# Performance work log

Hardware: AMD Instinct MI355X
Metric: run time of the kernel (lower is better)

The kernel has to match this reference:

```python
import jax, jax.numpy as jnp
import numpy as np

N_NODES = 100000
N_EDGES = 1600000
IN_CH = 128
HID = 64


def gcn_conv(x, W, b, src, dst, n):
    """PyG-style GCNConv: add self-loops, symmetric deg^-1/2 normalization."""
    h = x @ W  # [n, out]
    # degree including self-loop, computed from destination (col) indices
    deg = jax.ops.segment_sum(jnp.ones_like(dst, dtype=h.dtype), dst, num_segments=n) + 1.0
    dinv = jax.lax.rsqrt(deg)  # [n]
    norm = dinv[src] * dinv[dst]  # [E]
    agg = jax.ops.segment_sum(h[src] * norm[:, None], dst, num_segments=n)
    agg = agg + h * (1.0 / deg)[:, None]  # self-loop term: norm = 1/deg
    return agg + b


def setup_inputs() -> dict:
    key = jax.random.key(0)
    ks = jax.random.split(key, 6)
    x = jax.random.normal(ks[0], (N_NODES, IN_CH), dtype=jnp.float32)
    edge_index = jax.random.randint(ks[1], (2, N_EDGES), 0, N_NODES, dtype=jnp.int64)
    W1 = jax.random.normal(ks[2], (IN_CH, HID), dtype=jnp.float32) / np.sqrt(IN_CH)
    b1 = jnp.zeros((HID,), dtype=jnp.float32)
    W2 = jax.random.normal(ks[3], (HID, HID), dtype=jnp.float32) / np.sqrt(HID)
    b2 = jnp.zeros((HID,), dtype=jnp.float32)
    Wl = jax.random.normal(ks[4], (HID, 1), dtype=jnp.float32) / np.sqrt(HID)
    bl = jnp.zeros((1,), dtype=jnp.float32)
    return {"x": x, "edge_index": edge_index, "W1": W1, "b1": b1,
            "W2": W2, "b2": b2, "Wl": Wl, "bl": bl}


def reference(x, edge_index, W1, b1, W2, b2, Wl, bl):
    src, dst = edge_index[0], edge_index[1]
    n = x.shape[0]
    h = gcn_conv(x, W1, b1, src, dst, n)
    h = jax.nn.relu(h)
    # dropout: identity in eval mode
    h = gcn_conv(h, W2, b2, src, dst, n)
    h = jax.nn.relu(h)
    out = (h @ Wl + bl)[:, 0]  # [n]
    return out
```

## Files before the change

kernel.cpp:

```cpp
#include <hip/hip_runtime.h>
#include <hip/hip_fp16.h>


#define SHIFT 9
#define BSZ   (1 << SHIFT)
#define NBMAX 256
#define BIN_CH 1024
#define PMAX  11776

using f16x8 = __attribute__((ext_vector_type(8))) _Float16;
using f16x2 = __attribute__((ext_vector_type(2))) _Float16;
using f32x4 = __attribute__((ext_vector_type(4))) float;

__global__ __launch_bounds__(256) void k_bin(const int* __restrict__ src,
                                             const int* __restrict__ dst,
                                             unsigned* __restrict__ binned,
                                             int* __restrict__ gbase,
                                             __half* __restrict__ hs,
                                             int n, int nb, int E) {
    if (blockIdx.x == 0 && threadIdx.x < 8) {
        uint4 z = {0u, 0u, 0u, 0u};
        reinterpret_cast<uint4*>(hs + ((size_t)n << 6))[threadIdx.x] = z;
    }
    __shared__ int h[NBMAX];
    __shared__ int ex[NBMAX + 1];
    __shared__ int cur[NBMAX];
    __shared__ int stmp[256];
    const int t = threadIdx.x;
    const int blk = blockIdx.x;
    const int beg = blk * BIN_CH;
    for (int i = t; i < NBMAX; i += 256) h[i] = 0;
    __syncthreads();
    const int e4 = beg + t * 4;
    const bool act = e4 < E;
    int4 d4 = {0, 0, 0, 0};
    if (act) {
        d4 = *reinterpret_cast<const int4*>(dst + e4);
        atomicAdd(&h[d4.x >> SHIFT], 1);
        atomicAdd(&h[d4.y >> SHIFT], 1);
        atomicAdd(&h[d4.z >> SHIFT], 1);
        atomicAdd(&h[d4.w >> SHIFT], 1);
    }
    __syncthreads();
    const int hv = (t < nb) ? h[t] : 0;
    stmp[t] = hv;
    __syncthreads();
    for (int off = 1; off < 256; off <<= 1) {
        int u = (t >= off) ? stmp[t - off] : 0;
        __syncthreads();
        stmp[t] += u;
        __syncthreads();
    }
    if (t <= nb) ex[t] = stmp[t] - ((t < nb) ? h[t] : 0);
    __syncthreads();
    if (t < nb) cur[t] = ex[t];
    if (t <= nb) gbase[(size_t)blk * (nb + 1) + t] = ex[t];
    __syncthreads();
    if (act) {
        const int4 s4 = *reinterpret_cast<const int4*>(src + e4);
        int b0 = d4.x >> SHIFT, b1 = d4.y >> SHIFT;
        int b2 = d4.z >> SHIFT, b3 = d4.w >> SHIFT;
        int p0 = atomicAdd(&cur[b0], 1);
        int p1 = atomicAdd(&cur[b1], 1);
        int p2 = atomicAdd(&cur[b2], 1);
        int p3 = atomicAdd(&cur[b3], 1);
        binned[beg + p0] = (unsigned)s4.x | ((unsigned)(d4.x & (BSZ - 1)) << 17);
        binned[beg + p1] = (unsigned)s4.y | ((unsigned)(d4.y & (BSZ - 1)) << 17);
        binned[beg + p2] = (unsigned)s4.z | ((unsigned)(d4.z & (BSZ - 1)) << 17);
        binned[beg + p3] = (unsigned)s4.w | ((unsigned)(d4.w & (BSZ - 1)) << 17);
    }
}

#define TD 32
__global__ __launch_bounds__(256) void k_xpose(const int* __restrict__ gbase,
                                               int* __restrict__ gbaseT,
                                               int nblk, int nbp1) {
    __shared__ int tile[TD][TD + 1];
    const int ctiles = (nbp1 + TD - 1) / TD;
    const int bx = blockIdx.x % ctiles;
    const int by = blockIdx.x / ctiles;
    const int c0 = bx * TD, r0 = by * TD;
    const int tx = threadIdx.x & 31, ty = threadIdx.x >> 5;
    for (int dy = ty; dy < TD; dy += 8) {
        int r = r0 + dy, c = c0 + tx;
        tile[dy][tx] = (r < nblk && c < nbp1) ? gbase[(size_t)r * nbp1 + c] : 0;
    }
    __syncthreads();
    for (int dy = ty; dy < TD; dy += 8) {
        int r = c0 + dy, c = r0 + tx;
        if (r < nbp1 && c < nblk)
            gbaseT[(size_t)r * nblk + c] = tile[tx][dy];
    }
}

__global__ __launch_bounds__(1024) void k_bfill(const unsigned* __restrict__ binned,
                                                const int* __restrict__ gbaseT,
                                                int nblk, int nb,
                                                int* __restrict__ rowptr,
                                                int* __restrict__ colidx,
                                                float* __restrict__ dinv, int n) {
    __shared__ unsigned pedges[PMAX];
    __shared__ int segarr[2048];
    __shared__ int stmp[1024];
    __shared__ int cnt[BSZ];
    __shared__ int nbase[BSZ];
    const int b = blockIdx.x;
    const int t = threadIdx.x;
    const int* rowS = gbaseT + (size_t)b * nblk;
    const int* rowE = gbaseT + (size_t)(b + 1) * nblk;
    for (int i = t; i < BSZ; i += 1024) cnt[i] = 0;
    int eb = 0;
    {
        int l0 = 0, l1 = 0;
        if (t < nblk)        { int s0 = rowS[t];        l0 = rowE[t] - s0;        eb += s0; }
        if (t + 1024 < nblk) { int s0 = rowS[t + 1024]; l1 = rowE[t + 1024] - s0; eb += s0; }
        segarr[t] = l0;
        segarr[t + 1024] = l1;
    }
    stmp[t] = eb;
    __syncthreads();
    for (int off = 512; off; off >>= 1) {
        if (t < off) stmp[t] += stmp[t + off];
        __syncthreads();
    }
    const int ebeg = stmp[0];
    __syncthreads();
    const int a0 = segarr[2 * t];
    const int a1 = segarr[2 * t + 1];
    const int ps = a0 + a1;
    stmp[t] = ps;
    __syncthreads();
    for (int off = 1; off < 1024; off <<= 1) {
        int u = (t >= off) ? stmp[t - off] : 0;
        __syncthreads();
        stmp[t] += u;
        __syncthreads();
    }
    const int ecnt = min(stmp[1023], PMAX);
    const int exp2_ = stmp[t] - ps;
    segarr[2 * t] = exp2_;
    segarr[2 * t + 1] = exp2_ + a0;
    __syncthreads();
    for (int blk = t; blk < nblk; blk += 1024) {
        const int s0 = rowS[blk];
        const int c = rowE[blk] - s0;
        const int pos = segarr[blk];
        const unsigned* bp = binned + (size_t)blk * BIN_CH + s0;
        for (int k = 0; k < c; ++k) {
            const int d = pos + k;
            if (d < PMAX) pedges[d] = bp[k];
        }
    }
    __syncthreads();
    for (int j = t; j < ecnt; j += 1024)
        atomicAdd(&cnt[pedges[j] >> 17], 1);
    __syncthreads();
    const int c0 = (t < 256) ? cnt[2 * t] : 0;
    const int c1 = (t < 256) ? cnt[2 * t + 1] : 0;
    const int s2 = c0 + c1;
    stmp[t] = s2;
    __syncthreads();
    for (int off = 1; off < 256; off <<= 1) {
        int u = (t >= off && t < 256) ? stmp[t - off] : 0;
        __syncthreads();
        if (t < 256) stmp[t] += u;
        __syncthreads();
    }
    if (t < 256) {
        const int ex = stmp[t] - s2;
        nbase[2 * t] = ex;
        nbase[2 * t + 1] = ex + c0;
    }
    __syncthreads();
    const int gb9 = b << SHIFT;
    for (int j = t; j < BSZ; j += 1024) {
        const int g = gb9 + j;
        if (g < n) {
            rowptr[g] = (int)(((unsigned)(ebeg + nbase[j]) << 8) |
                              (unsigned)min(cnt[j], 255));
            dinv[g] = rsqrtf((float)cnt[j] + 1.0f);
        }
        cnt[j] = nbase[j];
    }
    __syncthreads();
    for (int j = t; j < ecnt; j += 1024) {
        const unsigned e = pedges[j];
        const int lo = (int)(e >> 17);
        const int off = atomicAdd(&cnt[lo], 1);
        colidx[ebeg + off] = (int)((e & 0x1FFFFu) << 7);
    }
}

template <int K, bool A_FP32>
__global__ __launch_bounds__(256) void k_gemm_mfma(const void* __restrict__ Av,
                                                   const float* __restrict__ W,
                                                   const float* __restrict__ dinv,
                                                   __half* __restrict__ C, int n) {
    constexpr int KP = K + 8;
    __shared__ _Float16 Wt[64 * KP];
    const int tid = threadIdx.x;
    for (int i = tid; i < K * 64; i += 256) {
        int k = i >> 6, c = i & 63;
        Wt[c * KP + k] = (_Float16)W[i];
    }
    __syncthreads();

    const int lane = tid & 63;
    const int wv = tid >> 6;
    const int r16 = lane & 15;
    const int kq = lane >> 4;
    const int rb = blockIdx.x * 64 + wv * 16;
    const int arow = min(rb + r16, n - 1);

    f32x4 acc[4] = {{0.f,0.f,0.f,0.f},{0.f,0.f,0.f,0.f},
                    {0.f,0.f,0.f,0.f},{0.f,0.f,0.f,0.f}};

#pragma unroll
    for (int kk = 0; kk < K; kk += 32) {
        f16x8 a;
        if (A_FP32) {
            const float* Ap = (const float*)Av + (size_t)arow * K + kk + kq * 8;
            float4 f0 = *reinterpret_cast<const float4*>(Ap);
            float4 f1 = *reinterpret_cast<const float4*>(Ap + 4);
            a[0] = (_Float16)f0.x; a[1] = (_Float16)f0.y;
            a[2] = (_Float16)f0.z; a[3] = (_Float16)f0.w;
            a[4] = (_Float16)f1.x; a[5] = (_Float16)f1.y;
            a[6] = (_Float16)f1.z; a[7] = (_Float16)f1.w;
        } else {
            const _Float16* Ap = (const _Float16*)Av + (size_t)arow * K + kk + kq * 8;
            a = *reinterpret_cast<const f16x8*>(Ap);
        }
#pragma unroll
        for (int nt = 0; nt < 4; ++nt) {
            f16x8 b = *reinterpret_cast<const f16x8*>(&Wt[(nt * 16 + r16) * KP + kk + kq * 8]);
            acc[nt] = __builtin_amdgcn_mfma_f32_16x16x32_f16(a, b, acc[nt], 0, 0, 0);
        }
    }

#pragma unroll
    for (int r = 0; r < 4; ++r) {
        const int row = rb + kq * 4 + r;
        if (row < n) {
            const float di = dinv[row];
#pragma unroll
            for (int nt = 0; nt < 4; ++nt)
                C[((size_t)row << 6) + nt * 16 + r16] = __float2half(acc[nt][r] * di);
        }
    }
}

__device__ __forceinline__ void dotu4(float acc[8], uint4 u, f16x2 pl, f16x2 ph) {
    union { uint4 u4; f16x2 h[4]; } v;
    v.u4 = u;
    acc[0] = __builtin_amdgcn_fdot2(v.h[0], pl, acc[0], false);
    acc[1] = __builtin_amdgcn_fdot2(v.h[0], ph, acc[1], false);
    acc[2] = __builtin_amdgcn_fdot2(v.h[1], pl, acc[2], false);
    acc[3] = __builtin_amdgcn_fdot2(v.h[1], ph, acc[3], false);
    acc[4] = __builtin_amdgcn_fdot2(v.h[2], pl, acc[4], false);
    acc[5] = __builtin_amdgcn_fdot2(v.h[2], ph, acc[5], false);
    acc[6] = __builtin_amdgcn_fdot2(v.h[3], pl, acc[6], false);
    acc[7] = __builtin_amdgcn_fdot2(v.h[3], ph, acc[7], false);
}

__device__ __forceinline__ void fold8(float acc[8]) {
#pragma unroll
    for (int m = 8; m <= 32; m <<= 1) {
#pragma unroll
        for (int j = 0; j < 8; ++j)
            acc[j] += __shfl_xor(acc[j], m, 64);
    }
}

__device__ __forceinline__ void gather_pair(const char* __restrict__ hsb,
                                            const int* __restrict__ colidx,
                                            unsigned pk0, unsigned pk1,
                                            int g, int p, unsigned dum,
                                            float acc0[8], float acc1[8]) {
    const f16x2 pl = {(_Float16)1.0f, (_Float16)0.0f};
    const f16x2 ph = {(_Float16)0.0f, (_Float16)1.0f};
    const int beg0 = (int)(pk0 >> 8), deg0 = (int)(pk0 & 255u);
    const int beg1 = (int)(pk1 >> 8), deg1 = (int)(pk1 & 255u);
    const int t0 = deg0 - g, t1 = deg1 - g;
    const unsigned poff = (unsigned)(p << 4);
    const unsigned dumo = dum + poff;
    const int ia = beg0 + g;
    const int ib = beg1 + g;
    unsigned a0 = (unsigned)colidx[ia]      + poff;
    unsigned a1 = (unsigned)colidx[ia + 8]  + poff;
    unsigned a2 = (unsigned)colidx[ia + 16] + poff;
    unsigned a3 = (unsigned)colidx[ia + 24] + poff;
    unsigned b0 = (unsigned)colidx[ib]      + poff;
    unsigned b1 = (unsigned)colidx[ib + 8]  + poff;
    unsigned b2 = (unsigned)colidx[ib + 16] + poff;
    unsigned b3 = (unsigned)colidx[ib + 24] + poff;
    unsigned oa0 = (0  < t0) ? a0 : dumo;
    unsigned oa1 = (8  < t0) ? a1 : dumo;
    unsigned oa2 = (16 < t0) ? a2 : dumo;
    unsigned oa3 = (24 < t0) ? a3 : dumo;
    unsigned ob0 = (0  < t1) ? b0 : dumo;
    unsigned ob1 = (8  < t1) ? b1 : dumo;
    unsigned ob2 = (16 < t1) ? b2 : dumo;
    unsigned ob3 = (24 < t1) ? b3 : dumo;
    uint4 ua0 = *reinterpret_cast<const uint4*>(hsb + oa0);
    uint4 ua1 = *reinterpret_cast<const uint4*>(hsb + oa1);
    uint4 ua2 = *reinterpret_cast<const uint4*>(hsb + oa2);
    uint4 ua3 = *reinterpret_cast<const uint4*>(hsb + oa3);
    uint4 ub0 = *reinterpret_cast<const uint4*>(hsb + ob0);
    uint4 ub1 = *reinterpret_cast<const uint4*>(hsb + ob1);
    uint4 ub2 = *reinterpret_cast<const uint4*>(hsb + ob2);
    uint4 ub3 = *reinterpret_cast<const uint4*>(hsb + ob3);
    dotu4(acc0, ua0, pl, ph);
    dotu4(acc0, ua1, pl, ph);
    dotu4(acc0, ua2, pl, ph);
    dotu4(acc0, ua3, pl, ph);
    dotu4(acc1, ub0, pl, ph);
    dotu4(acc1, ub1, pl, ph);
    dotu4(acc1, ub2, pl, ph);
    dotu4(acc1, ub3, pl, ph);
    const int ns0 = (deg0 + 7) >> 3;
    for (int k = 4; k < ns0; k += 4) {
        const int ik = beg0 + 8 * k + g;
        unsigned c0 = (unsigned)colidx[ik]      + poff;
        unsigned c1 = (unsigned)colidx[ik + 8]  + poff;
        unsigned c2 = (unsigned)colidx[ik + 16] + poff;
        unsigned c3 = (unsigned)colidx[ik + 24] + poff;
        const int kb = 8 * k;
        uint4 u0 = *reinterpret_cast<const uint4*>(hsb + ((kb      < t0) ? c0 : dumo));
        uint4 u1 = *reinterpret_cast<const uint4*>(hsb + ((kb + 8  < t0) ? c1 : dumo));
        uint4 u2 = *reinterpret_cast<const uint4*>(hsb + ((kb + 16 < t0) ? c2 : dumo));
        uint4 u3 = *reinterpret_cast<const uint4*>(hsb + ((kb + 24 < t0) ? c3 : dumo));
        dotu4(acc0, u0, pl, ph);
        dotu4(acc0, u1, pl, ph);
        dotu4(acc0, u2, pl, ph);
        dotu4(acc0, u3, pl, ph);
    }
    const int ns1 = (deg1 + 7) >> 3;
    for (int k = 4; k < ns1; k += 4) {
        const int ik = beg1 + 8 * k + g;
        unsigned c0 = (unsigned)colidx[ik]      + poff;
        unsigned c1 = (unsigned)colidx[ik + 8]  + poff;
        unsigned c2 = (unsigned)colidx[ik + 16] + poff;
        unsigned c3 = (unsigned)colidx[ik + 24] + poff;
        const int kb = 8 * k;
        uint4 u0 = *reinterpret_cast<const uint4*>(hsb + ((kb      < t1) ? c0 : dumo));
        uint4 u1 = *reinterpret_cast<const uint4*>(hsb + ((kb + 8  < t1) ? c1 : dumo));
        uint4 u2 = *reinterpret_cast<const uint4*>(hsb + ((kb + 16 < t1) ? c2 : dumo));
        uint4 u3 = *reinterpret_cast<const uint4*>(hsb + ((kb + 24 < t1) ? c3 : dumo));
        dotu4(acc1, u0, pl, ph);
        dotu4(acc1, u1, pl, ph);
        dotu4(acc1, u2, pl, ph);
        dotu4(acc1, u3, pl, ph);
    }
    fold8(acc0);
    fold8(acc1);
}

__global__ __launch_bounds__(256) void k_agg_relu(const __half* __restrict__ hs,
                                                  const int* __restrict__ rowptr,
                                                  const int* __restrict__ colidx,
                                                  const float* __restrict__ dinv,
                                                  const float* __restrict__ b,
                                                  __half* __restrict__ out, int n) {
    const int wv = threadIdx.x >> 6;
    const int i0 = blockIdx.x * 8 + wv * 2;
    const int lane = threadIdx.x & 63;
    if (i0 >= n) return;
    const int i1 = min(i0 + 1, n - 1);
    const int g = lane >> 3, p = lane & 7;
    const int iw = (lane & 8) ? i1 : i0;
    const unsigned pk0 = (unsigned)rowptr[i0];
    const unsigned pk1 = (unsigned)rowptr[i1];
    uint4 su = *reinterpret_cast<const uint4*>(hs + ((size_t)iw << 6) + (p << 3));
    const float di = dinv[iw];
    float acc0[8] = {}, acc1[8] = {};
    gather_pair((const char*)hs, colidx, pk0, pk1, g, p, (unsigned)n << 7,
                acc0, acc1);
    if (lane < 16) {
        const f16x2 pl = {(_Float16)1.0f, (_Float16)0.0f};
        const f16x2 ph = {(_Float16)0.0f, (_Float16)1.0f};
        float a[8];
#pragma unroll
        for (int j = 0; j < 8; ++j) a[j] = (lane & 8) ? acc1[j] : acc0[j];
        dotu4(a, su, pl, ph);
        float4 b0 = *reinterpret_cast<const float4*>(b + (p << 3));
        float4 b1 = *reinterpret_cast<const float4*>(b + (p << 3) + 4);
        __half2 h0 = __halves2half2(__float2half(fmaxf(fmaf(a[0], di, b0.x), 0.f)),
                                    __float2half(fmaxf(fmaf(a[1], di, b0.y), 0.f)));
        __half2 h1 = __halves2half2(__float2half(fmaxf(fmaf(a[2], di, b0.z), 0.f)),
                                    __float2half(fmaxf(fmaf(a[3], di, b0.w), 0.f)));
        __half2 h2 = __halves2half2(__float2half(fmaxf(fmaf(a[4], di, b1.x), 0.f)),
                                    __float2half(fmaxf(fmaf(a[5], di, b1.y), 0.f)));
        __half2 h3 = __halves2half2(__float2half(fmaxf(fmaf(a[6], di, b1.z), 0.f)),
                                    __float2half(fmaxf(fmaf(a[7], di, b1.w), 0.f)));
        uint4 u;
        u.x = *reinterpret_cast<unsigned*>(&h0);
        u.y = *reinterpret_cast<unsigned*>(&h1);
        u.z = *reinterpret_cast<unsigned*>(&h2);
        u.w = *reinterpret_cast<unsigned*>(&h3);
        if (iw < n && (i0 + 1 < n || !(lane & 8)))
            *reinterpret_cast<uint4*>(out + ((size_t)iw << 6) + (p << 3)) = u;
    }
}

__global__ __launch_bounds__(256) void k_agg_head(const __half* __restrict__ hs,
                                                  const int* __restrict__ rowptr,
                                                  const int* __restrict__ colidx,
                                                  const float* __restrict__ dinv,
                                                  const float* __restrict__ b2,
                                                  const float* __restrict__ Wl,
                                                  const float* __restrict__ bl,
                                                  float* __restrict__ out, int n) {
    const int wv = threadIdx.x >> 6;
    const int i0 = blockIdx.x * 8 + wv * 2;
    const int lane = threadIdx.x & 63;
    if (i0 >= n) return;
    const int i1 = min(i0 + 1, n - 1);
    const int g = lane >> 3, p = lane & 7;
    const int iw = (lane & 8) ? i1 : i0;
    const unsigned pk0 = (unsigned)rowptr[i0];
    const unsigned pk1 = (unsigned)rowptr[i1];
    uint4 su = *reinterpret_cast<const uint4*>(hs + ((size_t)iw << 6) + (p << 3));
    const float di = dinv[iw];
    float acc0[8] = {}, acc1[8] = {};
    gather_pair((const char*)hs, colidx, pk0, pk1, g, p, (unsigned)n << 7,
                acc0, acc1);
    const f16x2 pl = {(_Float16)1.0f, (_Float16)0.0f};
    const f16x2 ph = {(_Float16)0.0f, (_Float16)1.0f};
    float a[8];
#pragma unroll
    for (int j = 0; j < 8; ++j) a[j] = (lane & 8) ? acc1[j] : acc0[j];
    dotu4(a, su, pl, ph);
    float4 b0 = *reinterpret_cast<const float4*>(b2 + (p << 3));
    float4 b1 = *reinterpret_cast<const float4*>(b2 + (p << 3) + 4);
    float4 w0 = *reinterpret_cast<const float4*>(Wl + (p << 3));
    float4 w1 = *reinterpret_cast<const float4*>(Wl + (p << 3) + 4);
    float v = fmaxf(fmaf(a[0], di, b0.x), 0.f) * w0.x
            + fmaxf(fmaf(a[1], di, b0.y), 0.f) * w0.y
            + fmaxf(fmaf(a[2], di, b0.z), 0.f) * w0.z
            + fmaxf(fmaf(a[3], di, b0.w), 0.f) * w0.w
            + fmaxf(fmaf(a[4], di, b1.x), 0.f) * w1.x
            + fmaxf(fmaf(a[5], di, b1.y), 0.f) * w1.y
            + fmaxf(fmaf(a[6], di, b1.z), 0.f) * w1.z
            + fmaxf(fmaf(a[7], di, b1.w), 0.f) * w1.w;
    v += __shfl_xor(v, 1, 64);
    v += __shfl_xor(v, 2, 64);
    v += __shfl_xor(v, 4, 64);
    if (lane == 0) out[i0] = v + bl[0];
    if (lane == 8 && i0 + 1 < n) out[i1] = v + bl[0];
}

extern "C" void kernel_launch(void* const* d_in, const int* in_sizes, int n_in,
                              void* d_out, int out_size, void* d_ws, size_t ws_size,
                              hipStream_t stream) {
    const float* x  = (const float*)d_in[0];
    const int*   ei = (const int*)d_in[1];
    const float* W1 = (const float*)d_in[2];
    const float* b1 = (const float*)d_in[3];
    const float* W2 = (const float*)d_in[4];
    const float* b2 = (const float*)d_in[5];
    const float* Wl = (const float*)d_in[6];
    const float* bl = (const float*)d_in[7];
    float* out = (float*)d_out;

    const int n = in_sizes[0] / 128;
    const int E = in_sizes[1] / 2;
    const int* src = ei;
    const int* dst = ei + E;
    const int nb = (n + BSZ - 1) >> SHIFT;
    const int nblk = (E + BIN_CH - 1) / BIN_CH;

    char* ws = (char*)d_ws;
    size_t o = 0;
    auto alloc = [&](size_t bytes) {
        void* p = ws + o;
        o = (o + bytes + 255) & ~(size_t)255;
        return p;
    };
    float* dinv    = (float*)alloc((size_t)n * 4);
    int*   rowptr  = (int*)  alloc((size_t)(n + 1) * 4);
    int*   colidx  = (int*)  alloc(((size_t)E + 64) * 4);
    int*   gbase   = (int*)  alloc((size_t)nblk * (nb + 1) * 4);
    int*   gbaseT  = (int*)  alloc((size_t)(nb + 1) * nblk * 4);
    __half* hs     = (__half*)alloc((size_t)(n + 1) * 64 * 2);
    __half* bufA   = (__half*)alloc((size_t)n * 64 * 2);
    unsigned* binned = (unsigned*)alloc(((size_t)nblk * BIN_CH) * 4);

    k_bin<<<nblk, 256, 0, stream>>>(src, dst, binned, gbase, hs, n, nb, E);
    const int ctiles = (nb + 1 + TD - 1) / TD;
    const int rtiles = (nblk + TD - 1) / TD;
    k_xpose<<<ctiles * rtiles, 256, 0, stream>>>(gbase, gbaseT, nblk, nb + 1);
    k_bfill<<<nb, 1024, 0, stream>>>(binned, gbaseT, nblk, nb, rowptr, colidx,
                                     dinv, n);

    k_gemm_mfma<128, true><<<(n + 63) / 64, 256, 0, stream>>>(x, W1, dinv, hs, n);
    k_agg_relu<<<(n + 7) / 8, 256, 0, stream>>>(hs, rowptr, colidx, dinv, b1, bufA, n);

    k_gemm_mfma<64, false><<<(n + 63) / 64, 256, 0, stream>>>(bufA, W2, dinv, hs, n);
    k_agg_head<<<(n + 7) / 8, 256, 0, stream>>>(hs, rowptr, colidx, dinv, b2, Wl, bl,
                                                out, n);
}
```

Baseline: 133.1 us.

## Split aggregation by degree class, packing four low-degree nodes per wavefront

While building the CSR, nodes are classified into low-degree (<=16) and high-degree lists. Separate aggregation kernels then handle low-degree nodes four per wavefront, each with two gather slots per lane group, and high-degree nodes two per wavefront as before. The aim is to reduce wasted lanes and idle gather iterations for the many nodes with average degree around 16. The cost is extra global atomics and list writes in k_bfill, indirect node indexing that scatters output writes, and two more kernel launches sized for the worst case, whose extra blocks exit early.

```diff
diff --git a/kernel.cpp b/kernel.cpp
--- a/kernel.cpp
+++ b/kernel.cpp
@@ -17,10 +17,12 @@
                                              unsigned* __restrict__ binned,
                                              int* __restrict__ gbase,
                                              __half* __restrict__ hs,
+                                             int* __restrict__ clscnt,
                                              int n, int nb, int E) {
     if (blockIdx.x == 0 && threadIdx.x < 8) {
         uint4 z = {0u, 0u, 0u, 0u};
         reinterpret_cast<uint4*>(hs + ((size_t)n << 6))[threadIdx.x] = z;
+        if (threadIdx.x < 2) clscnt[threadIdx.x] = 0;
     }
     __shared__ int h[NBMAX];
     __shared__ int ex[NBMAX + 1];
@@ -98,17 +100,22 @@
                                                 int nblk, int nb,
                                                 int* __restrict__ rowptr,
                                                 int* __restrict__ colidx,
-                                                float* __restrict__ dinv, int n) {
+                                                float* __restrict__ dinv,
+                                                int* __restrict__ list0,
+                                                int* __restrict__ list1,
+                                                int* __restrict__ clscnt, int n) {
     __shared__ unsigned pedges[PMAX];
     __shared__ int segarr[2048];
     __shared__ int stmp[1024];
     __shared__ int cnt[BSZ];
     __shared__ int nbase[BSZ];
+    __shared__ int lcnt[2], lcur[2], lbase[2];
     const int b = blockIdx.x;
     const int t = threadIdx.x;
     const int* rowS = gbaseT + (size_t)b * nblk;
     const int* rowE = gbaseT + (size_t)(b + 1) * nblk;
     for (int i = t; i < BSZ; i += 1024) cnt[i] = 0;
+    if (t < 2) lcnt[t] = 0;
     int eb = 0;
     {
         int l0 = 0, l1 = 0;
@@ -176,9 +183,26 @@
     for (int j = t; j < BSZ; j += 1024) {
         const int g = gb9 + j;
         if (g < n) {
+            const int dg = cnt[j];
             rowptr[g] = (int)(((unsigned)(ebeg + nbase[j]) << 8) |
-                              (unsigned)min(cnt[j], 255));
-            dinv[g] = rsqrtf((float)cnt[j] + 1.0f);
+                              (unsigned)min(dg, 255));
+            dinv[g] = rsqrtf((float)dg + 1.0f);
+            atomicAdd(&lcnt[dg <= 16 ? 0 : 1], 1);
+        }
+    }
+    __syncthreads();
+    if (t < 2) {
+        lbase[t] = atomicAdd(&clscnt[t], lcnt[t]);
+        lcur[t] = 0;
+    }
+    __syncthreads();
+    for (int j = t; j < BSZ; j += 1024) {
+        const int g = gb9 + j;
+        if (g < n) {
+            const int dg = cnt[j];
+            const int c = dg <= 16 ? 0 : 1;
+            const int pos = atomicAdd(&lcur[c], 1);
+            (c ? list1 : list0)[lbase[c] + pos] = g;
         }
         cnt[j] = nbase[j];
     }
@@ -355,81 +379,96 @@
     fold8(acc1);
 }
 
-__global__ __launch_bounds__(256) void k_agg_relu(const __half* __restrict__ hs,
-                                                  const int* __restrict__ rowptr,
-                                                  const int* __restrict__ colidx,
-                                                  const float* __restrict__ dinv,
-                                                  const float* __restrict__ b,
-                                                  __half* __restrict__ out, int n) {
-    const int wv = threadIdx.x >> 6;
-    const int i0 = blockIdx.x * 8 + wv * 2;
-    const int lane = threadIdx.x & 63;
-    if (i0 >= n) return;
-    const int i1 = min(i0 + 1, n - 1);
-    const int g = lane >> 3, p = lane & 7;
-    const int iw = (lane & 8) ? i1 : i0;
-    const unsigned pk0 = (unsigned)rowptr[i0];
-    const unsigned pk1 = (unsigned)rowptr[i1];
-    uint4 su = *reinterpret_cast<const uint4*>(hs + ((size_t)iw << 6) + (p << 3));
-    const float di = dinv[iw];
-    float acc0[8] = {}, acc1[8] = {};
-    gather_pair((const char*)hs, colidx, pk0, pk1, g, p, (unsigned)n << 7,
-                acc0, acc1);
-    if (lane < 16) {
-        const f16x2 pl = {(_Float16)1.0f, (_Float16)0.0f};
-        const f16x2 ph = {(_Float16)0.0f, (_Float16)1.0f};
-        float a[8];
-#pragma unroll
-        for (int j = 0; j < 8; ++j) a[j] = (lane & 8) ? acc1[j] : acc0[j];
-        dotu4(a, su, pl, ph);
-        float4 b0 = *reinterpret_cast<const float4*>(b + (p << 3));
-        float4 b1 = *reinterpret_cast<const float4*>(b + (p << 3) + 4);
-        __half2 h0 = __halves2half2(__float2half(fmaxf(fmaf(a[0], di, b0.x), 0.f)),
-                                    __float2half(fmaxf(fmaf(a[1], di, b0.y), 0.f)));
-        __half2 h1 = __halves2half2(__float2half(fmaxf(fmaf(a[2], di, b0.z), 0.f)),
-                                    __float2half(fmaxf(fmaf(a[3], di, b0.w), 0.f)));
-        __half2 h2 = __halves2half2(__float2half(fmaxf(fmaf(a[4], di, b1.x), 0.f)),
-                                    __float2half(fmaxf(fmaf(a[5], di, b1.y), 0.f)));
-        __half2 h3 = __halves2half2(__float2half(fmaxf(fmaf(a[6], di, b1.z), 0.f)),
-                                    __float2half(fmaxf(fmaf(a[7], di, b1.w), 0.f)));
-        uint4 u;
-        u.x = *reinterpret_cast<unsigned*>(&h0);
-        u.y = *reinterpret_cast<unsigned*>(&h1);
-        u.z = *reinterpret_cast<unsigned*>(&h2);
-        u.w = *reinterpret_cast<unsigned*>(&h3);
-        if (iw < n && (i0 + 1 < n || !(lane & 8)))
-            *reinterpret_cast<uint4*>(out + ((size_t)iw << 6) + (p << 3)) = u;
-    }
-}
-
-__global__ __launch_bounds__(256) void k_agg_head(const __half* __restrict__ hs,
-                                                  const int* __restrict__ rowptr,
-                                                  const int* __restrict__ colidx,
-                                                  const float* __restrict__ dinv,
-                                                  const float* __restrict__ b2,
-                                                  const float* __restrict__ Wl,
-                                                  const float* __restrict__ bl,
-                                                  float* __restrict__ out, int n) {
-    const int wv = threadIdx.x >> 6;
-    const int i0 = blockIdx.x * 8 + wv * 2;
-    const int lane = threadIdx.x & 63;
-    if (i0 >= n) return;
-    const int i1 = min(i0 + 1, n - 1);
-    const int g = lane >> 3, p = lane & 7;
-    const int iw = (lane & 8) ? i1 : i0;
-    const unsigned pk0 = (unsigned)rowptr[i0];
-    const unsigned pk1 = (unsigned)rowptr[i1];
-    uint4 su = *reinterpret_cast<const uint4*>(hs + ((size_t)iw << 6) + (p << 3));
-    const float di = dinv[iw];
-    float acc0[8] = {}, acc1[8] = {};
-    gather_pair((const char*)hs, colidx, pk0, pk1, g, p, (unsigned)n << 7,
-                acc0, acc1);
+__device__ __forceinline__ void gather_quad2(const char* __restrict__ hsb,
+                                             const int* __restrict__ colidx,
+                                             unsigned pk0, unsigned pk1,
+                                             unsigned pk2, unsigned pk3,
+                                             int g, int p, unsigned dum,
+                                             float a0[8], float a1[8],
+                                             float a2[8], float a3[8]) {
     const f16x2 pl = {(_Float16)1.0f, (_Float16)0.0f};
     const f16x2 ph = {(_Float16)0.0f, (_Float16)1.0f};
-    float a[8];
-#pragma unroll
-    for (int j = 0; j < 8; ++j) a[j] = (lane & 8) ? acc1[j] : acc0[j];
-    dotu4(a, su, pl, ph);
+    const int beg0 = (int)(pk0 >> 8), deg0 = (int)(pk0 & 255u);
+    const int beg1 = (int)(pk1 >> 8), deg1 = (int)(pk1 & 255u);
+    const int beg2 = (int)(pk2 >> 8), deg2 = (int)(pk2 & 255u);
+    const int beg3 = (int)(pk3 >> 8), deg3 = (int)(pk3 & 255u);
+    const int t0 = deg0 - g, t1 = deg1 - g, t2 = deg2 - g, t3 = deg3 - g;
+    const unsigned poff = (unsigned)(p << 4);
+    const unsigned dumo = dum + poff;
+    const int ia = beg0 + g, ib = beg1 + g, ic = beg2 + g, id = beg3 + g;
+    unsigned a_0 = (unsigned)colidx[ia]     + poff;
+    unsigned a_1 = (unsigned)colidx[ia + 8] + poff;
+    unsigned b_0 = (unsigned)colidx[ib]     + poff;
+    unsigned b_1 = (unsigned)colidx[ib + 8] + poff;
+    unsigned c_0 = (unsigned)colidx[ic]     + poff;
+    unsigned c_1 = (unsigned)colidx[ic + 8] + poff;
+    unsigned d_0 = (unsigned)colidx[id]     + poff;
+    unsigned d_1 = (unsigned)colidx[id + 8] + poff;
+    unsigned oa0 = (0 < t0) ? a_0 : dumo;
+    unsigned oa1 = (8 < t0) ? a_1 : dumo;
+    unsigned ob0 = (0 < t1) ? b_0 : dumo;
+    unsigned ob1 = (8 < t1) ? b_1 : dumo;
+    unsigned oc0 = (0 < t2) ? c_0 : dumo;
+    unsigned oc1 = (8 < t2) ? c_1 : dumo;
+    unsigned od0 = (0 < t3) ? d_0 : dumo;
+    unsigned od1 = (8 < t3) ? d_1 : dumo;
+    uint4 ua0 = *reinterpret_cast<const uint4*>(hsb + oa0);
+    uint4 ua1 = *reinterpret_cast<const uint4*>(hsb + oa1);
+    uint4 ub0 = *reinterpret_cast<const uint4*>(hsb + ob0);
+    uint4 ub1 = *reinterpret_cast<const uint4*>(hsb + ob1);
+    uint4 uc0 = *reinterpret_cast<const uint4*>(hsb + oc0);
+    uint4 uc1 = *reinterpret_cast<const uint4*>(hsb + oc1);
+    uint4 ud0 = *reinterpret_cast<const uint4*>(hsb + od0);
+    uint4 ud1 = *reinterpret_cast<const uint4*>(hsb + od1);
+    dotu4(a0, ua0, pl, ph);
+    dotu4(a0, ua1, pl, ph);
+    dotu4(a1, ub0, pl, ph);
+    dotu4(a1, ub1, pl, ph);
+    dotu4(a2, uc0, pl, ph);
+    dotu4(a2, uc1, pl, ph);
+    dotu4(a3, ud0, pl, ph);
+    dotu4(a3, ud1, pl, ph);
+    fold8(a0);
+    fold8(a1);
+    fold8(a2);
+    fold8(a3);
+}
+
+__device__ __forceinline__ void sel4(float a[8], int nsel, const float a0[8],
+                                     const float a1[8], const float a2[8],
+                                     const float a3[8]) {
+#pragma unroll
+    for (int j = 0; j < 8; ++j) {
+        float x01 = (nsel & 1) ? a1[j] : a0[j];
+        float x23 = (nsel & 1) ? a3[j] : a2[j];
+        a[j] = (nsel & 2) ? x23 : x01;
+    }
+}
+
+__device__ __forceinline__ void store_relu(float a[8], float di,
+                                           const float* __restrict__ b, int p,
+                                           __half* __restrict__ out, int row) {
+    float4 b0 = *reinterpret_cast<const float4*>(b + (p << 3));
+    float4 b1 = *reinterpret_cast<const float4*>(b + (p << 3) + 4);
+    __half2 h0 = __halves2half2(__float2half(fmaxf(fmaf(a[0], di, b0.x), 0.f)),
+                                __float2half(fmaxf(fmaf(a[1], di, b0.y), 0.f)));
+    __half2 h1 = __halves2half2(__float2half(fmaxf(fmaf(a[2], di, b0.z), 0.f)),
+                                __float2half(fmaxf(fmaf(a[3], di, b0.w), 0.f)));
+    __half2 h2 = __halves2half2(__float2half(fmaxf(fmaf(a[4], di, b1.x), 0.f)),
+                                __float2half(fmaxf(fmaf(a[5], di, b1.y), 0.f)));
+    __half2 h3 = __halves2half2(__float2half(fmaxf(fmaf(a[6], di, b1.z), 0.f)),
+                                __float2half(fmaxf(fmaf(a[7], di, b1.w), 0.f)));
+    uint4 u;
+    u.x = *reinterpret_cast<unsigned*>(&h0);
+    u.y = *reinterpret_cast<unsigned*>(&h1);
+    u.z = *reinterpret_cast<unsigned*>(&h2);
+    u.w = *reinterpret_cast<unsigned*>(&h3);
+    *reinterpret_cast<uint4*>(out + ((size_t)row << 6) + (p << 3)) = u;
+}
+
+__device__ __forceinline__ float head_val(float a[8], float di,
+                                          const float* __restrict__ b2,
+                                          const float* __restrict__ Wl, int p) {
     float4 b0 = *reinterpret_cast<const float4*>(b2 + (p << 3));
     float4 b1 = *reinterpret_cast<const float4*>(b2 + (p << 3) + 4);
     float4 w0 = *reinterpret_cast<const float4*>(Wl + (p << 3));
@@ -445,8 +484,162 @@
     v += __shfl_xor(v, 1, 64);
     v += __shfl_xor(v, 2, 64);
     v += __shfl_xor(v, 4, 64);
-    if (lane == 0) out[i0] = v + bl[0];
-    if (lane == 8 && i0 + 1 < n) out[i1] = v + bl[0];
+    return v;
+}
+
+__global__ __launch_bounds__(256) void k_agg_relu_c0(const __half* __restrict__ hs,
+                                                     const int* __restrict__ rowptr,
+                                                     const int* __restrict__ colidx,
+                                                     const int* __restrict__ list,
+                                                     const int* __restrict__ clscnt,
+                                                     const float* __restrict__ dinv,
+                                                     const float* __restrict__ b,
+                                                     __half* __restrict__ out, int n) {
+    const int cntc = clscnt[0];
+    const int i0 = (blockIdx.x * 4 + (threadIdx.x >> 6)) * 4;
+    if (i0 >= cntc) return;
+    const int lane = threadIdx.x & 63;
+    const int g = lane >> 3, p = lane & 7;
+    const int nsel = g & 3;
+    const int last = cntc - 1;
+    const int id0 = list[min(i0,     last)];
+    const int id1 = list[min(i0 + 1, last)];
+    const int id2 = list[min(i0 + 2, last)];
+    const int id3 = list[min(i0 + 3, last)];
+    const int idsel = (nsel & 1) ? ((nsel & 2) ? id3 : id1)
+                                 : ((nsel & 2) ? id2 : id0);
+    const bool valid = (i0 + nsel) < cntc;
+    const unsigned pk0 = (unsigned)rowptr[id0];
+    const unsigned pk1 = (unsigned)rowptr[id1];
+    const unsigned pk2 = (unsigned)rowptr[id2];
+    const unsigned pk3 = (unsigned)rowptr[id3];
+    uint4 su = *reinterpret_cast<const uint4*>(hs + ((size_t)idsel << 6) + (p << 3));
+    const float di = dinv[idsel];
+    float a0[8] = {}, a1[8] = {}, a2[8] = {}, a3[8] = {};
+    gather_quad2((const char*)hs, colidx, pk0, pk1, pk2, pk3, g, p,
+                 (unsigned)n << 7, a0, a1, a2, a3);
+    if (lane < 32 && valid) {
+        const f16x2 pl = {(_Float16)1.0f, (_Float16)0.0f};
+        const f16x2 ph = {(_Float16)0.0f, (_Float16)1.0f};
+        float a[8];
+        sel4(a, nsel, a0, a1, a2, a3);
+        dotu4(a, su, pl, ph);
+        store_relu(a, di, b, p, out, idsel);
+    }
+}
+
+__global__ __launch_bounds__(256) void k_agg_relu_c1(const __half* __restrict__ hs,
+                                                     const int* __restrict__ rowptr,
+                                                     const int* __restrict__ colidx,
+                                                     const int* __restrict__ list,
+                                                     const int* __restrict__ clscnt,
+                                                     const float* __restrict__ dinv,
+                                                     const float* __restrict__ b,
+                                                     __half* __restrict__ out, int n) {
+    const int cntc = clscnt[1];
+    const int i0 = (blockIdx.x * 4 + (threadIdx.x >> 6)) * 2;
+    if (i0 >= cntc) return;
+    const int lane = threadIdx.x & 63;
+    const int g = lane >> 3, p = lane & 7;
+    const int last = cntc - 1;
+    const int id0 = list[min(i0,     last)];
+    const int id1 = list[min(i0 + 1, last)];
+    const int iw = (lane & 8) ? id1 : id0;
+    const bool valid = (i0 + ((lane >> 3) & 1)) < cntc;
+    const unsigned pk0 = (unsigned)rowptr[id0];
+    const unsigned pk1 = (unsigned)rowptr[id1];
+    uint4 su = *reinterpret_cast<const uint4*>(hs + ((size_t)iw << 6) + (p << 3));
+    const float di = dinv[iw];
+    float acc0[8] = {}, acc1[8] = {};
+    gather_pair((const char*)hs, colidx, pk0, pk1, g, p, (unsigned)n << 7,
+                acc0, acc1);
+    if (lane < 16 && valid) {
+        const f16x2 pl = {(_Float16)1.0f, (_Float16)0.0f};
+        const f16x2 ph = {(_Float16)0.0f, (_Float16)1.0f};
+        float a[8];
+#pragma unroll
+        for (int j = 0; j < 8; ++j) a[j] = (lane & 8) ? acc1[j] : acc0[j];
+        dotu4(a, su, pl, ph);
+        store_relu(a, di, b, p, out, iw);
+    }
+}
+
+__global__ __launch_bounds__(256) void k_agg_head_c0(const __half* __restrict__ hs,
+                                                     const int* __restrict__ rowptr,
+                                                     const int* __restrict__ colidx,
+                                                     const int* __restrict__ list,
+                                                     const int* __restrict__ clscnt,
+                                                     const float* __restrict__ dinv,
+                                                     const float* __restrict__ b2,
+                                                     const float* __restrict__ Wl,
+                                                     const float* __restrict__ bl,
+                                                     float* __restrict__ out, int n) {
+    const int cntc = clscnt[0];
+    const int i0 = (blockIdx.x * 4 + (threadIdx.x >> 6)) * 4;
+    if (i0 >= cntc) return;
+    const int lane = threadIdx.x & 63;
+    const int g = lane >> 3, p = lane & 7;
+    const int nsel = g & 3;
+    const int last = cntc - 1;
+    const int id0 = list[min(i0,     last)];
+    const int id1 = list[min(i0 + 1, last)];
+    const int id2 = list[min(i0 + 2, last)];
+    const int id3 = list[min(i0 + 3, last)];
+    const int idsel = (nsel & 1) ? ((nsel & 2) ? id3 : id1)
+                                 : ((nsel & 2) ? id2 : id0);
+    const unsigned pk0 = (unsigned)rowptr[id0];
+    const unsigned pk1 = (unsigned)rowptr[id1];
+    const unsigned pk2 = (unsigned)rowptr[id2];
+    const unsigned pk3 = (unsigned)rowptr[id3];
+    uint4 su = *reinterpret_cast<const uint4*>(hs + ((size_t)idsel << 6) + (p << 3));
+    const float di = dinv[idsel];
+    float a0[8] = {}, a1[8] = {}, a2[8] = {}, a3[8] = {};
+    gather_quad2((const char*)hs, colidx, pk0, pk1, pk2, pk3, g, p,
+                 (unsigned)n << 7, a0, a1, a2, a3);
+    const f16x2 pl = {(_Float16)1.0f, (_Float16)0.0f};
+    const f16x2 ph = {(_Float16)0.0f, (_Float16)1.0f};
+    float a[8];
+    sel4(a, nsel, a0, a1, a2, a3);
+    dotu4(a, su, pl, ph);
+    const float v = head_val(a, di, b2, Wl, p);
+    if (p == 0 && g < 4 && (i0 + g) < cntc) out[idsel] = v + bl[0];
+}
+
+__global__ __launch_bounds__(256) void k_agg_head_c1(const __half* __restrict__ hs,
+                                                     const int* __restrict__ rowptr,
+                                                     const int* __restrict__ colidx,
+                                                     const int* __restrict__ list,
+                                                     const int* __restrict__ clscnt,
+                                                     const float* __restrict__ dinv,
+                                                     const float* __restrict__ b2,
+                                                     const float* __restrict__ Wl,
+                                                     const float* __restrict__ bl,
+                                                     float* __restrict__ out, int n) {
+    const int cntc = clscnt[1];
+    const int i0 = (blockIdx.x * 4 + (threadIdx.x >> 6)) * 2;
+    if (i0 >= cntc) return;
+    const int lane = threadIdx.x & 63;
+    const int g = lane >> 3, p = lane & 7;
+    const int last = cntc - 1;
+    const int id0 = list[min(i0,     last)];
+    const int id1 = list[min(i0 + 1, last)];
+    const int iw = (lane & 8) ? id1 : id0;
+    const unsigned pk0 = (unsigned)rowptr[id0];
+    const unsigned pk1 = (unsigned)rowptr[id1];
+    uint4 su = *reinterpret_cast<const uint4*>(hs + ((size_t)iw << 6) + (p << 3));
+    const float di = dinv[iw];
+    float acc0[8] = {}, acc1[8] = {};
+    gather_pair((const char*)hs, colidx, pk0, pk1, g, p, (unsigned)n << 7,
+                acc0, acc1);
+    const f16x2 pl = {(_Float16)1.0f, (_Float16)0.0f};
+    const f16x2 ph = {(_Float16)0.0f, (_Float16)1.0f};
+    float a[8];
+#pragma unroll
+    for (int j = 0; j < 8; ++j) a[j] = (lane & 8) ? acc1[j] : acc0[j];
+    dotu4(a, su, pl, ph);
+    const float v = head_val(a, di, b2, Wl, p);
+    if (lane == 0) out[id0] = v + bl[0];
+    if (lane == 8 && i0 + 1 < cntc) out[id1] = v + bl[0];
 }
 
 extern "C" void kernel_launch(void* const* d_in, const int* in_sizes, int n_in,
@@ -481,21 +674,31 @@
     int*   colidx  = (int*)  alloc(((size_t)E + 64) * 4);
     int*   gbase   = (int*)  alloc((size_t)nblk * (nb + 1) * 4);
     int*   gbaseT  = (int*)  alloc((size_t)(nb + 1) * nblk * 4);
+    int*   list0   = (int*)  alloc((size_t)n * 4);
+    int*   list1   = (int*)  alloc((size_t)n * 4);
+    int*   clscnt  = (int*)  alloc(256);
     __half* hs     = (__half*)alloc((size_t)(n + 1) * 64 * 2);
     __half* bufA   = (__half*)alloc((size_t)n * 64 * 2);
     unsigned* binned = (unsigned*)alloc(((size_t)nblk * BIN_CH) * 4);
 
-    k_bin<<<nblk, 256, 0, stream>>>(src, dst, binned, gbase, hs, n, nb, E);
+    k_bin<<<nblk, 256, 0, stream>>>(src, dst, binned, gbase, hs, clscnt, n, nb, E);
     const int ctiles = (nb + 1 + TD - 1) / TD;
     const int rtiles = (nblk + TD - 1) / TD;
     k_xpose<<<ctiles * rtiles, 256, 0, stream>>>(gbase, gbaseT, nblk, nb + 1);
     k_bfill<<<nb, 1024, 0, stream>>>(binned, gbaseT, nblk, nb, rowptr, colidx,
-                                     dinv, n);
+                                     dinv, list0, list1, clscnt, n);
 
     k_gemm_mfma<128, true><<<(n + 63) / 64, 256, 0, stream>>>(x, W1, dinv, hs, n);
-    k_agg_relu<<<(n + 7) / 8, 256, 0, stream>>>(hs, rowptr, colidx, dinv, b1, bufA, n);
+    k_agg_relu_c0<<<(n + 15) / 16, 256, 0, stream>>>(hs, rowptr, colidx, list0,
+                                                     clscnt, dinv, b1, bufA, n);
+    k_agg_relu_c1<<<(n + 7) / 8, 256, 0, stream>>>(hs, rowptr, colidx, list1,
+                                                   clscnt, dinv, b1, bufA, n);
 
     k_gemm_mfma<64, false><<<(n + 63) / 64, 256, 0, stream>>>(bufA, W2, dinv, hs, n);
-    k_agg_head<<<(n + 7) / 8, 256, 0, stream>>>(hs, rowptr, colidx, dinv, b2, Wl, bl,
-                                                out, n);
-}
+    k_agg_head_c0<<<(n + 15) / 16, 256, 0, stream>>>(hs, rowptr, colidx, list0,
+                                                     clscnt, dinv, b2, Wl, bl,
+                                                     out, n);
+    k_agg_head_c1<<<(n + 7) / 8, 256, 0, stream>>>(hs, rowptr, colidx, list1,
+                                                   clscnt, dinv, b2, Wl, bl,
+                                                   out, n);
+}
```

Measured after the change: 147.9 us. 1.11x slower.
